# Kernel optimization log

Measured on AMD Instinct MI355X. Metric: run time of the kernel, lower is better.

Reference implementation:

```python
import jax, jax.numpy as jnp
import numpy as np

D = 256; NH = 8; NL = 4; NP = 4; NLAYERS = 6; DFF = 1024; DH = D // NH
B = 2
SHAPES = [(128, 128), (64, 64), (32, 32), (16, 16)]
S_TOTAL = sum(h * w for h, w in SHAPES)  # 21760


def setup_inputs() -> dict:
    key = jax.random.key(0)
    ks = iter(jax.random.split(key, 64))
    inp = {}
    for l, (h, w) in enumerate(SHAPES):
        inp[f"src{l}"] = jax.random.normal(next(ks), (B, D, h, w), jnp.float32)
        inp[f"pos{l}"] = jax.random.normal(next(ks), (B, D, h, w), jnp.float32)
    def p(shape):
        return jax.random.normal(next(ks), shape, jnp.float32) * 0.02
    inp["level_embed"] = p((NL, D))
    inp["Woff"] = p((NLAYERS, D, NH * NL * NP * 2)); inp["boff"] = p((NLAYERS, NH * NL * NP * 2))
    inp["Wattn"] = p((NLAYERS, D, NH * NL * NP)); inp["battn"] = p((NLAYERS, NH * NL * NP))
    inp["Wval"] = p((NLAYERS, D, D)); inp["bval"] = p((NLAYERS, D))
    inp["Wout"] = p((NLAYERS, D, D)); inp["bout"] = p((NLAYERS, D))
    inp["ln1_s"] = jnp.ones((NLAYERS, D)); inp["ln1_b"] = jnp.zeros((NLAYERS, D))
    inp["W1"] = p((NLAYERS, D, DFF)); inp["b1"] = p((NLAYERS, DFF))
    inp["W2"] = p((NLAYERS, DFF, D)); inp["b2"] = p((NLAYERS, D))
    inp["ln2_s"] = jnp.ones((NLAYERS, D)); inp["ln2_b"] = jnp.zeros((NLAYERS, D))
    return inp


def _layer_norm(x, s, b, eps=1e-5):
    m = jnp.mean(x, -1, keepdims=True)
    v = jnp.mean((x - m) ** 2, -1, keepdims=True)
    return (x - m) * jax.lax.rsqrt(v + eps) * s + b


def _ref_points(batch):
    # masks are all-False -> valid_ratios == 1, so reference points are just
    # normalized pixel centers, identical across the level axis.
    refs = []
    for h, w in SHAPES:
        yy, xx = jnp.meshgrid((jnp.arange(h) + 0.5) / h, (jnp.arange(w) + 0.5) / w, indexing="ij")
        refs.append(jnp.stack([xx.ravel(), yy.ravel()], -1))
    ref = jnp.concatenate(refs, 0)  # [S, 2] (x, y)
    return jnp.broadcast_to(ref[None, :, None, :], (batch, S_TOTAL, NL, 2))


def _ms_deform_attn(query, ref, src, Woff, boff, Wattn, battn, Wval, bval, Wout, bout):
    Bq, S, _ = query.shape
    value = (src @ Wval + bval).reshape(Bq, S, NH, DH)
    off = (query @ Woff + boff).reshape(Bq, S, NH, NL, NP, 2)
    aw = jax.nn.softmax((query @ Wattn + battn).reshape(Bq, S, NH, NL * NP), -1)
    aw = aw.reshape(Bq, S, NH, NL, NP)
    norm = jnp.array([[w, h] for h, w in SHAPES], dtype=query.dtype)  # [NL,2] = (W,H)
    loc = ref[:, :, None, :, None, :] + off / norm[None, None, None, :, None, :]  # [B,S,NH,NL,NP,2]
    out = jnp.zeros((Bq, NH, S, DH), query.dtype)
    start = 0
    for l, (h, w) in enumerate(SHAPES):
        v = value[:, start:start + h * w].transpose(0, 2, 1, 3)  # [B,NH,h*w,DH]
        start += h * w
        # grid_sample align_corners=False convention
        x = loc[:, :, :, l, :, 0] * w - 0.5  # [B,S,NH,NP]
        y = loc[:, :, :, l, :, 1] * h - 0.5
        x0 = jnp.floor(x); y0 = jnp.floor(y)
        lx = x - x0; ly = y - y0
        x0i = x0.astype(jnp.int32); y0i = y0.astype(jnp.int32)
        def tr(a):  # [B,S,NH,NP] -> [B,NH,S*NP,1]
            return a.transpose(0, 2, 1, 3).reshape(Bq, NH, S * NP, 1)
        def gather(xi, yi):
            ok = (xi >= 0) & (xi < w) & (yi >= 0) & (yi < h)
            idx = jnp.clip(yi, 0, h - 1) * w + jnp.clip(xi, 0, w - 1)
            idx = idx.transpose(0, 2, 1, 3).reshape(Bq, NH, S * NP)
            g = jnp.take_along_axis(v, idx[..., None], axis=2)  # [B,NH,S*NP,DH]
            return g * tr(ok).astype(v.dtype)  # zero padding outside
        samp = (tr((1 - lx) * (1 - ly)) * gather(x0i, y0i)
                + tr(lx * (1 - ly)) * gather(x0i + 1, y0i)
                + tr((1 - lx) * ly) * gather(x0i, y0i + 1)
                + tr(lx * ly) * gather(x0i + 1, y0i + 1))
        samp = (samp * tr(aw[:, :, :, l])).reshape(Bq, NH, S, NP, DH).sum(3)
        out = out + samp
    out = out.transpose(0, 2, 1, 3).reshape(Bq, S, D)
    return out @ Wout + bout


def _forward(srcs, poss, level_embed, Woff, boff, Wattn, battn, Wval, bval, Wout, bout,
             ln1_s, ln1_b, W1, b1, W2, b2, ln2_s, ln2_b):
    bsz = srcs[0].shape[0]
    src_flat = jnp.concatenate([s.reshape(bsz, D, -1).transpose(0, 2, 1) for s in srcs], 1)
    pos_flat = jnp.concatenate(
        [p.reshape(bsz, D, -1).transpose(0, 2, 1) + level_embed[l] for l, p in enumerate(poss)], 1)
    ref = _ref_points(bsz)
    out = src_flat
    for i in range(NLAYERS):
        q = out + pos_flat
        attn = _ms_deform_attn(q, ref, out, Woff[i], boff[i], Wattn[i], battn[i],
                               Wval[i], bval[i], Wout[i], bout[i])
        out = _layer_norm(out + attn, ln1_s[i], ln1_b[i])
        ff = jax.nn.relu(out @ W1[i] + b1[i]) @ W2[i] + b2[i]
        out = _layer_norm(out + ff, ln2_s[i], ln2_b[i])
    return out  # memory: [B, S_TOTAL, D]


def reference(src0, src1, src2, src3, pos0, pos1, pos2, pos3, level_embed,
              Woff, boff, Wattn, battn, Wval, bval, Wout, bout,
              ln1_s, ln1_b, W1, b1, W2, b2, ln2_s, ln2_b):
    return _forward([src0, src1, src2, src3], [pos0, pos1, pos2, pos3], level_embed,
                    Woff, boff, Wattn, battn, Wval, bval, Wout, bout,
                    ln1_s, ln1_b, W1, b1, W2, b2, ln2_s, ln2_b)
```

## Files before the change

### kernel.cpp

```cpp
#include <hip/hip_runtime.h>
#include <math.h>

#define DMODEL 256
#define NHEADS 8
#define NLAY 6
#define DFF 1024
#define DHEAD 32
#define NB 2
#define STOT 21760
#define MTOT (NB * STOT)

typedef unsigned short u16;
typedef __attribute__((ext_vector_type(8))) short short8;
typedef __attribute__((ext_vector_type(4))) float floatx4;
typedef __attribute__((ext_vector_type(2))) float float2v;

__device__ __forceinline__ float bf2f(u16 h) {
    unsigned int u = ((unsigned int)h) << 16;
    return __uint_as_float(u);
}
__device__ __forceinline__ u16 f2bf(float f) {
    unsigned int u = __float_as_uint(f);
    u = u + 0x7fffu + ((u >> 16) & 1u);
    return (u16)(u >> 16);
}

__device__ __forceinline__ void pkfma(float2v& acc, float2v a, float2v b) {
    asm("v_pk_fma_f32 %0, %1, %2, %0" : "+v"(acc) : "v"(a), "v"(b));
}
__device__ __forceinline__ float2v unpk(unsigned int u) {
    float2v r;
    r.x = __uint_as_float(u << 16);
    r.y = __uint_as_float(u & 0xffff0000u);
    return r;
}

__device__ __forceinline__ void gload16(const u16* g, u16* l) {
    __builtin_amdgcn_global_load_lds(
        (const __attribute__((address_space(1))) unsigned int*)(g),
        (__attribute__((address_space(3))) unsigned int*)(l),
        16, 0, 0);
}

__global__ __launch_bounds__(256)
void biascat_kernel(const float* __restrict__ boff, const float* __restrict__ battn,
                    float* __restrict__ bias384)
{
    const int t = blockIdx.x * 256 + threadIdx.x;
    if (t >= NLAY * 384) return;
    const int i = t / 384, c = t - i * 384;
    bias384[t] = (c < 256) ? boff[i * 256 + c] : battn[i * 128 + (c - 256)];
}

__global__ __launch_bounds__(256)
void wtrans_kernel(const float* __restrict__ W, u16* __restrict__ Wt,
                   const int K, const int N, const long wstride, const long ostride)
{
    __shared__ float ts[32][33];
    W  += blockIdx.z * wstride;
    Wt += blockIdx.z * ostride;
    const int n0 = blockIdx.x * 32;
    const int k0 = blockIdx.y * 32;
    const int t = threadIdx.x;
    const int nl = t & 31, kl = t >> 5;
#pragma unroll
    for (int p = 0; p < 4; ++p) {
        const int k = kl + p * 8;
        ts[k][nl] = W[(long)(k0 + k) * N + n0 + nl];
    }
    __syncthreads();
    const int c = t & 31, r0 = t >> 5;
#pragma unroll
    for (int p = 0; p < 4; ++p) {
        const int r = r0 + p * 8;
        Wt[(long)(n0 + r) * K + k0 + c] = f2bf(ts[c][r]);
    }
}

__global__ __launch_bounds__(256)
void flatten_kernel(const float* __restrict__ src, const float* __restrict__ pos,
                    const float* __restrict__ le_row,
                    float* __restrict__ out, u16* __restrict__ outb,
                    u16* __restrict__ posb, u16* __restrict__ qb,
                    int HW, int start)
{
    __shared__ float ts[32][33];
    __shared__ float tp[32][33];
    const int b   = blockIdx.z;
    const int d0  = blockIdx.y * 32;
    const int hw0 = blockIdx.x * 32;
    const int t   = threadIdx.x;
    const int hwl = t & 31;
    const int dl  = t >> 5;
#pragma unroll
    for (int p = 0; p < 4; ++p) {
        const int dd = dl + p * 8;
        const int d  = d0 + dd;
        const long idx = ((long)(b * DMODEL + d)) * HW + hw0 + hwl;
        ts[dd][hwl] = src[idx];
        tp[dd][hwl] = pos[idx] + le_row[d];
    }
    __syncthreads();
    const int dl2  = t & 31;
    const int hwl2 = t >> 5;
#pragma unroll
    for (int p = 0; p < 4; ++p) {
        const int hh  = hwl2 + p * 8;
        const int tok = start + hw0 + hh;
        const long o  = ((long)(b * STOT + tok)) * DMODEL + d0 + dl2;
        const float v = ts[dl2][hh];
        const float pp = tp[dl2][hh];
        out[o]  = v;
        outb[o] = f2bf(v);
        posb[o] = f2bf(pp);
        qb[o]   = f2bf(v + pp);
    }
}

__global__ __launch_bounds__(256)
void mfma_gemm(const u16* __restrict__ A, const u16* __restrict__ Bt,
               const int ldb, const float* __restrict__ bias,
               u16* __restrict__ Cb, const int ldc, u16* __restrict__ Cb2,
               const int K, const int relu)
{
    __shared__ u16 As[2][128 * 32];
    __shared__ u16 Bs[2][128 * 32];
    const int tid  = threadIdx.x;
    const int wv   = tid >> 6;
    const int lane = tid & 63;
    const int m0 = blockIdx.y * 128;
    const int n0 = blockIdx.x * 128;
    const int wm = (wv & 1) * 64;
    const int wn = (wv >> 1) * 64;
    const int q   = lane >> 4;
    const int c16 = lane & 15;

    const int lrow = lane >> 2;
    const int lcol = (lane & 3) * 8;

    const u16* ag[2];
    const u16* bg[2];
#pragma unroll
    for (int it = 0; it < 2; ++it) {
        const int chunk = it * 4 + wv;
        const int row = chunk * 16 + lrow;
        ag[it] = A  + (long)(m0 + row) * K   + lcol;
        bg[it] = Bt + (long)(n0 + row) * ldb + lcol;
    }

#define STAGE(buf, kk)                                          \
    {                                                           \
        _Pragma("unroll")                                       \
        for (int it = 0; it < 2; ++it) {                        \
            const int chunk = it * 4 + wv;                      \
            gload16(ag[it] + (kk), &As[buf][chunk * 512]);      \
            gload16(bg[it] + (kk), &Bs[buf][chunk * 512]);      \
        }                                                       \
    }

    floatx4 acc[4][4];
#pragma unroll
    for (int i = 0; i < 4; ++i)
#pragma unroll
        for (int j = 0; j < 4; ++j)
            acc[i][j] = (floatx4){0.f, 0.f, 0.f, 0.f};

    STAGE(0, 0);
    __syncthreads();

    int cur = 0;
    for (int k0 = 0; k0 < K; k0 += 32) {
        const int nxt = k0 + 32;
        if (nxt < K) {
            if (cur) { STAGE(0, nxt); } else { STAGE(1, nxt); }
        }

        const u16* Ab = &As[cur][0];
        const u16* Bb = &Bs[cur][0];
        short8 af[4], bf[4];
#pragma unroll
        for (int i = 0; i < 4; ++i) {
            af[i] = *(const short8*)&Ab[(wm + i * 16 + c16) * 32 + q * 8];
            bf[i] = *(const short8*)&Bb[(wn + i * 16 + c16) * 32 + q * 8];
        }
#pragma unroll
        for (int i = 0; i < 4; ++i)
#pragma unroll
            for (int j = 0; j < 4; ++j)
                acc[i][j] = __builtin_amdgcn_mfma_f32_16x16x32_bf16(
                    af[i], bf[j], acc[i][j], 0, 0, 0);
        __syncthreads();
        cur ^= 1;
    }
#undef STAGE

    u16* cb  = Cb;
    int ldcb = ldc, csub = 0;
    if (Cb2 && n0 >= 256) { cb = Cb2; ldcb = 128; csub = 256; }

#pragma unroll
    for (int i = 0; i < 4; ++i) {
#pragma unroll
        for (int j = 0; j < 4; ++j) {
            const int col = n0 + wn + j * 16 + c16;
            const float bv = bias ? bias[col] : 0.f;
#pragma unroll
            for (int r = 0; r < 4; ++r) {
                const int row = m0 + wm + i * 16 + q * 4 + r;
                float v = acc[i][j][r] + bv;
                if (relu) v = fmaxf(v, 0.f);
                cb[(long)row * ldcb + col - csub] = f2bf(v);
            }
        }
    }
}

__device__ __forceinline__ void point_corners(
    float refx, float refy, unsigned int o2, float aP,
    int k, unsigned int base, float* w, unsigned int* o)
{
    const int lw = 128 >> k;
    const float flw = (float)lw;
    const float x = refx * flw - 0.5f + bf2f((u16)(o2 & 0xffffu));
    const float y = refy * flw - 0.5f + bf2f((u16)(o2 >> 16));
    const float x0f = floorf(x), y0f = floorf(y);
    const float lx = x - x0f, ly = y - y0f;
    const int x0 = (int)x0f, y0 = (int)y0f;
    const float wx0 = ((unsigned int)x0 < (unsigned int)lw) ? (1.f - lx) : 0.f;
    const float wx1 = ((unsigned int)(x0 + 1) < (unsigned int)lw) ? lx : 0.f;
    const float wy0 = ((unsigned int)y0 < (unsigned int)lw) ? (aP * (1.f - ly)) : 0.f;
    const float wy1 = ((unsigned int)(y0 + 1) < (unsigned int)lw) ? (aP * ly) : 0.f;
    const unsigned int xc0 = (unsigned int)(x0 & (lw - 1)) << 9;
    const unsigned int xc1 = (unsigned int)((x0 + 1) & (lw - 1)) << 9;
    const unsigned int r0 = (unsigned int)(y0 & (lw - 1)) << (16 - k);
    const unsigned int r1 = (unsigned int)((y0 + 1) & (lw - 1)) << (16 - k);
    w[0] = wy0 * wx0; o[0] = base + r0 + xc0;
    w[1] = wy0 * wx1; o[1] = base + r0 + xc1;
    w[2] = wy1 * wx0; o[2] = base + r1 + xc0;
    w[3] = wy1 * wx1; o[3] = base + r1 + xc1;
}

__global__ __launch_bounds__(256, 4)
void sample_kernel(const u16* __restrict__ value, const u16* __restrict__ offb,
                   const u16* __restrict__ logit, u16* __restrict__ sb)
{
    __shared__ unsigned int pwtab[4 * 8 * 132];

    const int t  = threadIdx.x;
    const int wv = t >> 6;
    const int l  = t & 63;
    const int h  = l >> 3;
    const int u  = l & 7;
    const int blk = blockIdx.x * 4 + wv;
    const int b = blk / STOT;
    const int s = blk - b * STOT;

    float refx, refy;
    if (s < 16384) {
        const int yy = s >> 7, xx = s & 127;
        refx = (xx + 0.5f) * (1.f / 128.f); refy = (yy + 0.5f) * (1.f / 128.f);
    } else if (s < 20480) {
        const int sl = s - 16384; const int yy = sl >> 6, xx = sl & 63;
        refx = (xx + 0.5f) * (1.f / 64.f);  refy = (yy + 0.5f) * (1.f / 64.f);
    } else if (s < 21504) {
        const int sl = s - 20480; const int yy = sl >> 5, xx = sl & 31;
        refx = (xx + 0.5f) * (1.f / 32.f);  refy = (yy + 0.5f) * (1.f / 32.f);
    } else {
        const int sl = s - 21504; const int yy = sl >> 4, xx = sl & 15;
        refx = (xx + 0.5f) * (1.f / 16.f);  refy = (yy + 0.5f) * (1.f / 16.f);
    }

    const unsigned int* offp = (const unsigned int*)(offb + (long)blk * 256 + h * 32);
    const unsigned int o2_0 = offp[u];
    const unsigned int o2_1 = offp[u + 8];
    const u16* lp = logit + (long)blk * 128 + h * 16;
    const float l0 = bf2f(lp[u]);
    const float l1 = bf2f(lp[u + 8]);

    float m = fmaxf(l0, l1);
    m = fmaxf(m, __shfl_xor(m, 1));
    m = fmaxf(m, __shfl_xor(m, 2));
    m = fmaxf(m, __shfl_xor(m, 4));
    const float e0 = __expf(l0 - m);
    const float e1 = __expf(l1 - m);
    float se = e0 + e1;
    se += __shfl_xor(se, 1);
    se += __shfl_xor(se, 2);
    se += __shfl_xor(se, 4);
    const float inv = 1.f / se;
    const float aP0 = e0 * inv;
    const float aP1 = e1 * inv;

    const int k0 = u >> 2;
    const unsigned int LS0 = k0 ? 16384u : 0u;
    const unsigned int LS1 = k0 ? 21504u : 20480u;
    const unsigned int tb = (unsigned int)(b * STOT);
    const unsigned int hb64 = (unsigned int)(h * 64);
    const unsigned int base0 = (tb + LS0) * 512u + hb64;
    const unsigned int base1 = (tb + LS1) * 512u + hb64;

    float ww[8];
    unsigned int oo[8];
    point_corners(refx, refy, o2_0, aP0, k0,     base0, ww,     oo);
    point_corners(refx, refy, o2_1, aP1, k0 + 2, base1, ww + 4, oo + 4);

    unsigned int* wbase = pwtab + (wv * 8 + h) * 132;
    {
        uint4 p0, p1, p2, p3;
        p0.x = __float_as_uint(ww[0]); p0.y = oo[0];
        p0.z = __float_as_uint(ww[1]); p0.w = oo[1];
        p1.x = __float_as_uint(ww[2]); p1.y = oo[2];
        p1.z = __float_as_uint(ww[3]); p1.w = oo[3];
        p2.x = __float_as_uint(ww[4]); p2.y = oo[4];
        p2.z = __float_as_uint(ww[5]); p2.w = oo[5];
        p3.x = __float_as_uint(ww[6]); p3.y = oo[6];
        p3.z = __float_as_uint(ww[7]); p3.w = oo[7];
        *(uint4*)(wbase + u * 8)           = p0;
        *(uint4*)(wbase + u * 8 + 4)       = p1;
        *(uint4*)(wbase + (u + 8) * 8)     = p2;
        *(uint4*)(wbase + (u + 8) * 8 + 4) = p3;
    }
    __builtin_amdgcn_wave_barrier();

    const unsigned int chb = (unsigned int)(u * 8);
    const char* vp = (const char*)value;
    float2v acc0; acc0.x = 0.f; acc0.y = 0.f;
    float2v acc1; acc1.x = 0.f; acc1.y = 0.f;

#pragma unroll
    for (int g = 0; g < 4; ++g) {
        const uint4* gp = (const uint4*)(wbase + g * 32);
        uint4 qq[8];
#pragma unroll
        for (int i = 0; i < 8; ++i) qq[i] = gp[i];
        uint2 dB[16];
#pragma unroll
        for (int i = 0; i < 8; ++i) {
            dB[2 * i]     = *(const uint2*)(vp + (qq[i].y + chb));
            dB[2 * i + 1] = *(const uint2*)(vp + (qq[i].w + chb));
        }
#pragma unroll
        for (int i = 0; i < 8; ++i) {
            float2v wa; wa.x = __uint_as_float(qq[i].x); wa.y = wa.x;
            pkfma(acc0, wa, unpk(dB[2 * i].x));
            pkfma(acc1, wa, unpk(dB[2 * i].y));
            float2v wb; wb.x = __uint_as_float(qq[i].z); wb.y = wb.x;
            pkfma(acc0, wb, unpk(dB[2 * i + 1].x));
            pkfma(acc1, wb, unpk(dB[2 * i + 1].y));
        }
    }

    ushort4 r;
    r.x = f2bf(acc0.x); r.y = f2bf(acc0.y);
    r.z = f2bf(acc1.x); r.w = f2bf(acc1.y);
    *(ushort4*)(sb + (long)blk * DMODEL + h * 32 + u * 4) = r;
}

__global__ __launch_bounds__(256)
void ln_kernel(float* __restrict__ out, u16* __restrict__ outb,
               u16* __restrict__ qb, const u16* __restrict__ posb,
               const u16* __restrict__ db,
               const float* __restrict__ gamma, const float* __restrict__ beta)
{
    const int wave = threadIdx.x >> 6;
    const int lane = threadIdx.x & 63;
    const long tok = (long)blockIdx.x * 4 + wave;
    float* op = out + tok * DMODEL + lane * 4;
    const float4 xo = *(const float4*)op;
    const ushort4 d4 = *(const ushort4*)(db + tok * DMODEL + lane * 4);
    float x[4] = {xo.x + bf2f(d4.x), xo.y + bf2f(d4.y),
                  xo.z + bf2f(d4.z), xo.w + bf2f(d4.w)};

    float sum = x[0] + x[1] + x[2] + x[3];
#pragma unroll
    for (int o = 32; o >= 1; o >>= 1) sum += __shfl_xor(sum, o);
    const float mean = sum * (1.f / 256.f);

    float vs = 0.f;
#pragma unroll
    for (int i = 0; i < 4; ++i) { const float d2 = x[i] - mean; vs += d2 * d2; }
#pragma unroll
    for (int o = 32; o >= 1; o >>= 1) vs += __shfl_xor(vs, o);
    const float rstd = rsqrtf(vs * (1.f / 256.f) + 1e-5f);

    const float4 g  = *(const float4*)(gamma + lane * 4);
    const float4 be = *(const float4*)(beta + lane * 4);
    float r[4];
    r[0] = (x[0] - mean) * rstd * g.x + be.x;
    r[1] = (x[1] - mean) * rstd * g.y + be.y;
    r[2] = (x[2] - mean) * rstd * g.z + be.z;
    r[3] = (x[3] - mean) * rstd * g.w + be.w;
    float4 rf; rf.x = r[0]; rf.y = r[1]; rf.z = r[2]; rf.w = r[3];
    *(float4*)op = rf;
    ushort4 rb;
    rb.x = f2bf(r[0]); rb.y = f2bf(r[1]); rb.z = f2bf(r[2]); rb.w = f2bf(r[3]);
    *(ushort4*)(outb + tok * DMODEL + lane * 4) = rb;
    if (qb) {
        const ushort4 p4 = *(const ushort4*)(posb + tok * DMODEL + lane * 4);
        ushort4 qv;
        qv.x = f2bf(r[0] + bf2f(p4.x));
        qv.y = f2bf(r[1] + bf2f(p4.y));
        qv.z = f2bf(r[2] + bf2f(p4.z));
        qv.w = f2bf(r[3] + bf2f(p4.w));
        *(ushort4*)(qb + tok * DMODEL + lane * 4) = qv;
    }
}

extern "C" void kernel_launch(void* const* d_in, const int* in_sizes, int n_in,
                              void* d_out, int out_size, void* d_ws, size_t ws_size,
                              hipStream_t stream)
{
    const float* src[4] = {(const float*)d_in[0], (const float*)d_in[2],
                           (const float*)d_in[4], (const float*)d_in[6]};
    const float* pos[4] = {(const float*)d_in[1], (const float*)d_in[3],
                           (const float*)d_in[5], (const float*)d_in[7]};
    const float* level_embed = (const float*)d_in[8];
    const float* Woff  = (const float*)d_in[9];
    const float* boff  = (const float*)d_in[10];
    const float* Wattn = (const float*)d_in[11];
    const float* battn = (const float*)d_in[12];
    const float* Wval  = (const float*)d_in[13];
    const float* bval  = (const float*)d_in[14];
    const float* Wout  = (const float*)d_in[15];
    const float* bout  = (const float*)d_in[16];
    const float* ln1s  = (const float*)d_in[17];
    const float* ln1b  = (const float*)d_in[18];
    const float* W1    = (const float*)d_in[19];
    const float* b1    = (const float*)d_in[20];
    const float* W2    = (const float*)d_in[21];
    const float* b2    = (const float*)d_in[22];
    const float* ln2s  = (const float*)d_in[23];
    const float* ln2b  = (const float*)d_in[24];

    float* out = (float*)d_out;
    const long MD = (long)MTOT * DMODEL;

    u16* outb = (u16*)d_ws;
    u16* posb = outb + MD;
    u16* qb   = posb + MD;
    u16* db   = qb + MD;
    u16* vb   = db + MD;
    u16* offb = vb + MD;
    u16* awb  = offb + MD;
    u16* sb   = awb + MD / 2;
    u16* hb   = vb;
    u16* wts  = vb + 4 * MD;
    u16* Wvalt = wts;
    u16* Wofat = Wvalt + 6L * 256 * 256;
    u16* Woutt = Wofat + 6L * 384 * 256;
    u16* W1t   = Woutt + 6L * 256 * 256;
    u16* W2t   = W1t   + 6L * 1024 * 256;
    float* bias384 = (float*)(W2t + 6L * 1024 * 256);

    biascat_kernel<<<9, 256, 0, stream>>>(boff, battn, bias384);
    wtrans_kernel<<<dim3(8, 8, 6),  256, 0, stream>>>(Wval,  Wvalt, 256, 256,
                                                      65536, 65536);
    wtrans_kernel<<<dim3(8, 8, 6),  256, 0, stream>>>(Woff,  Wofat, 256, 256,
                                                      65536, 98304);
    wtrans_kernel<<<dim3(4, 8, 6),  256, 0, stream>>>(Wattn, Wofat + 256 * 256,
                                                      256, 128, 32768, 98304);
    wtrans_kernel<<<dim3(8, 8, 6),  256, 0, stream>>>(Wout,  Woutt, 256, 256,
                                                      65536, 65536);
    wtrans_kernel<<<dim3(32, 8, 6), 256, 0, stream>>>(W1,    W1t, 256, 1024,
                                                      262144, 262144);
    wtrans_kernel<<<dim3(8, 32, 6), 256, 0, stream>>>(W2,    W2t, 1024, 256,
                                                      262144, 262144);

    {
        const int HW[4] = {16384, 4096, 1024, 256};
        const int ST[4] = {0, 16384, 20480, 21504};
        for (int l = 0; l < 4; ++l) {
            dim3 g(HW[l] / 32, DMODEL / 32, NB);
            flatten_kernel<<<g, 256, 0, stream>>>(src[l], pos[l],
                                                  level_embed + l * DMODEL,
                                                  out, outb, posb, qb, HW[l], ST[l]);
        }
    }

    const dim3 g2(2, MTOT / 128);
    const dim3 g3(3, MTOT / 128);
    const dim3 g8(8, MTOT / 128);

    for (int i = 0; i < NLAY; ++i) {
        const u16* Wv  = Wvalt + (long)i * 256 * 256;
        const u16* Wqa = Wofat + (long)i * 384 * 256;
        const u16* Wou = Woutt + (long)i * 256 * 256;
        const u16* W1i = W1t   + (long)i * 1024 * 256;
        const u16* W2i = W2t   + (long)i * 256 * 1024;
        const float* bv  = bval + (long)i * 256;
        const float* bqa = bias384 + (long)i * 384;
        const float* bou = bout + (long)i * 256;
        const float* b1i = b1   + (long)i * DFF;
        const float* b2i = b2   + (long)i * 256;

        mfma_gemm<<<g2, 256, 0, stream>>>(outb, Wv, 256, bv,
                                          vb, 256, nullptr, 256, 0);
        mfma_gemm<<<g3, 256, 0, stream>>>(qb, Wqa, 256, bqa,
                                          offb, 256, awb, 256, 0);
        sample_kernel<<<MTOT / 4, 256, 0, stream>>>(vb, offb, awb, sb);
        mfma_gemm<<<g2, 256, 0, stream>>>(sb, Wou, 256, bou,
                                          db, 256, nullptr, 256, 0);
        ln_kernel<<<MTOT / 4, 256, 0, stream>>>(out, outb, nullptr, nullptr, db,
                                                ln1s + (long)i * 256,
                                                ln1b + (long)i * 256);
        mfma_gemm<<<g8, 256, 0, stream>>>(outb, W1i, 256, b1i,
                                          hb, 1024, nullptr, 256, 1);
        mfma_gemm<<<g2, 256, 0, stream>>>(hb, W2i, 1024, b2i,
                                          db, 256, nullptr, 1024, 0);
        ln_kernel<<<MTOT / 4, 256, 0, stream>>>(out, outb, qb, posb, db,
                                                ln2s + (long)i * 256,
                                                ln2b + (long)i * 256);
    }
}
```

Measured before the change: 1.900 ms.

## Merge value and offset GEMMs into one launch; software-pipeline sampling gathers

The value projection and the offset/attention-logit projection now run as a single grouped GEMM launch: blocks with column index past a split point switch to the second operand set. This removes one launch per layer and fills the GPU better with 5 column tiles instead of 2 and 3. The sampling kernel double-buffers its gather loads so the next group's value loads are in flight while the current group is accumulated, with sched_barriers enforcing the order. This raises register use, so occupancy is lowered from 4 to 3 blocks per CU.

```diff
diff --git a/kernel.cpp b/kernel.cpp
--- a/kernel.cpp
+++ b/kernel.cpp
@@ -121,15 +121,22 @@
 void mfma_gemm(const u16* __restrict__ A, const u16* __restrict__ Bt,
                const int ldb, const float* __restrict__ bias,
                u16* __restrict__ Cb, const int ldc, u16* __restrict__ Cb2,
-               const int K, const int relu)
+               const int K, const int relu,
+               const u16* __restrict__ A1, const u16* __restrict__ Bt1,
+               const float* __restrict__ bias1, u16* __restrict__ Cb1,
+               u16* __restrict__ Cb21, const int nsplit)
 {
     __shared__ u16 As[2][128 * 32];
     __shared__ u16 Bs[2][128 * 32];
+    int bx = blockIdx.x;
+    if (A1 && bx >= nsplit) {
+        A = A1; Bt = Bt1; bias = bias1; Cb = Cb1; Cb2 = Cb21; bx -= nsplit;
+    }
     const int tid  = threadIdx.x;
     const int wv   = tid >> 6;
     const int lane = tid & 63;
     const int m0 = blockIdx.y * 128;
-    const int n0 = blockIdx.x * 128;
+    const int n0 = bx * 128;
     const int wm = (wv & 1) * 64;
     const int wn = (wv >> 1) * 64;
     const int q   = lane >> 4;
@@ -240,7 +247,34 @@
     w[3] = wy1 * wx1; o[3] = base + r1 + xc1;
 }
 
-__global__ __launch_bounds__(256, 4)
+#define LDQ(Q, g)                                                   \
+    {                                                               \
+        const uint4* gp_ = (const uint4*)(wbase + (g) * 32);        \
+        _Pragma("unroll")                                           \
+        for (int i = 0; i < 8; ++i) Q[i] = gp_[i];                  \
+    }
+#define GATH(D, Q)                                                  \
+    {                                                               \
+        _Pragma("unroll")                                           \
+        for (int i = 0; i < 8; ++i) {                               \
+            D[2 * i]     = *(const uint2*)(vp + (Q[i].y + chb));    \
+            D[2 * i + 1] = *(const uint2*)(vp + (Q[i].w + chb));    \
+        }                                                           \
+    }
+#define FMAG(D, Q)                                                  \
+    {                                                               \
+        _Pragma("unroll")                                           \
+        for (int i = 0; i < 8; ++i) {                               \
+            float2v wa; wa.x = __uint_as_float(Q[i].x); wa.y = wa.x;\
+            pkfma(acc0, wa, unpk(D[2 * i].x));                      \
+            pkfma(acc1, wa, unpk(D[2 * i].y));                      \
+            float2v wb; wb.x = __uint_as_float(Q[i].z); wb.y = wb.x;\
+            pkfma(acc0, wb, unpk(D[2 * i + 1].x));                  \
+            pkfma(acc1, wb, unpk(D[2 * i + 1].y));                  \
+        }                                                           \
+    }
+
+__global__ __launch_bounds__(256, 3)
 void sample_kernel(const u16* __restrict__ value, const u16* __restrict__ offb,
                    const u16* __restrict__ logit, u16* __restrict__ sb)
 {
@@ -327,28 +361,23 @@
     float2v acc0; acc0.x = 0.f; acc0.y = 0.f;
     float2v acc1; acc1.x = 0.f; acc1.y = 0.f;
 
-#pragma unroll
-    for (int g = 0; g < 4; ++g) {
-        const uint4* gp = (const uint4*)(wbase + g * 32);
-        uint4 qq[8];
-#pragma unroll
-        for (int i = 0; i < 8; ++i) qq[i] = gp[i];
-        uint2 dB[16];
-#pragma unroll
-        for (int i = 0; i < 8; ++i) {
-            dB[2 * i]     = *(const uint2*)(vp + (qq[i].y + chb));
-            dB[2 * i + 1] = *(const uint2*)(vp + (qq[i].w + chb));
-        }
-#pragma unroll
-        for (int i = 0; i < 8; ++i) {
-            float2v wa; wa.x = __uint_as_float(qq[i].x); wa.y = wa.x;
-            pkfma(acc0, wa, unpk(dB[2 * i].x));
-            pkfma(acc1, wa, unpk(dB[2 * i].y));
-            float2v wb; wb.x = __uint_as_float(qq[i].z); wb.y = wb.x;
-            pkfma(acc0, wb, unpk(dB[2 * i + 1].x));
-            pkfma(acc1, wb, unpk(dB[2 * i + 1].y));
-        }
-    }
+    uint4 qA[8], qB[8];
+    uint2 dA[16], dB[16];
+
+    LDQ(qA, 0); GATH(dA, qA);
+    LDQ(qB, 1); GATH(dB, qB);
+    __builtin_amdgcn_sched_barrier(0);
+    FMAG(dA, qA);
+    __builtin_amdgcn_sched_barrier(0);
+    LDQ(qA, 2); GATH(dA, qA);
+    __builtin_amdgcn_sched_barrier(0);
+    FMAG(dB, qB);
+    __builtin_amdgcn_sched_barrier(0);
+    LDQ(qB, 3); GATH(dB, qB);
+    __builtin_amdgcn_sched_barrier(0);
+    FMAG(dA, qA);
+    __builtin_amdgcn_sched_barrier(0);
+    FMAG(dB, qB);
 
     ushort4 r;
     r.x = f2bf(acc0.x); r.y = f2bf(acc0.y);
@@ -478,7 +507,7 @@
     }
 
     const dim3 g2(2, MTOT / 128);
-    const dim3 g3(3, MTOT / 128);
+    const dim3 g5(5, MTOT / 128);
     const dim3 g8(8, MTOT / 128);
 
     for (int i = 0; i < NLAY; ++i) {
@@ -493,20 +522,25 @@
         const float* b1i = b1   + (long)i * DFF;
         const float* b2i = b2   + (long)i * 256;
 
-        mfma_gemm<<<g2, 256, 0, stream>>>(outb, Wv, 256, bv,
-                                          vb, 256, nullptr, 256, 0);
-        mfma_gemm<<<g3, 256, 0, stream>>>(qb, Wqa, 256, bqa,
-                                          offb, 256, awb, 256, 0);
+        mfma_gemm<<<g5, 256, 0, stream>>>(outb, Wv, 256, bv,
+                                          vb, 256, nullptr, 256, 0,
+                                          qb, Wqa, bqa, offb, awb, 2);
         sample_kernel<<<MTOT / 4, 256, 0, stream>>>(vb, offb, awb, sb);
         mfma_gemm<<<g2, 256, 0, stream>>>(sb, Wou, 256, bou,
-                                          db, 256, nullptr, 256, 0);
+                                          db, 256, nullptr, 256, 0,
+                                          nullptr, nullptr, nullptr, nullptr,
+                                          nullptr, 0);
         ln_kernel<<<MTOT / 4, 256, 0, stream>>>(out, outb, nullptr, nullptr, db,
                                                 ln1s + (long)i * 256,
                                                 ln1b + (long)i * 256);
         mfma_gemm<<<g8, 256, 0, stream>>>(outb, W1i, 256, b1i,
-                                          hb, 1024, nullptr, 256, 1);
+                                          hb, 1024, nullptr, 256, 1,
+                                          nullptr, nullptr, nullptr, nullptr,
+                                          nullptr, 0);
         mfma_gemm<<<g2, 256, 0, stream>>>(hb, W2i, 1024, b2i,
-                                          db, 256, nullptr, 1024, 0);
+                                          db, 256, nullptr, 1024, 0,
+                                          nullptr, nullptr, nullptr, nullptr,
+                                          nullptr, 0);
         ln_kernel<<<MTOT / 4, 256, 0, stream>>>(out, outb, qb, posb, db,
                                                 ln2s + (long)i * 256,
                                                 ln2b + (long)i * 256);
```

Result: faster. 1.861 ms (-2.1%).

## Triple-buffer GEMM k-loop with single barrier and merge value/offset GEMM launches

Applied to the files above, without the earlier changes.

The GEMM main loop moves from double to triple buffering. It keeps two stages of async global-to-LDS loads in flight, uses explicit vmcnt waits, and needs only one barrier per k-step. The kernel also gains a second operand set selected by block x index, so the value projection and the offset/attention projection run in one launch. This raises LDS use per block, which may lower occupancy, and adds hand-written waitcnt assembly that depends on the load count per stage.

```diff
diff --git a/kernel.cpp b/kernel.cpp
--- a/kernel.cpp
+++ b/kernel.cpp
@@ -121,15 +121,22 @@
 void mfma_gemm(const u16* __restrict__ A, const u16* __restrict__ Bt,
                const int ldb, const float* __restrict__ bias,
                u16* __restrict__ Cb, const int ldc, u16* __restrict__ Cb2,
-               const int K, const int relu)
-{
-    __shared__ u16 As[2][128 * 32];
-    __shared__ u16 Bs[2][128 * 32];
+               const int K, const int relu,
+               const u16* __restrict__ A1, const u16* __restrict__ Bt1,
+               const float* __restrict__ bias1, u16* __restrict__ Cb1,
+               u16* __restrict__ Cb21, const int nsplit)
+{
+    __shared__ u16 As[3][128 * 32];
+    __shared__ u16 Bs[3][128 * 32];
+    int bx = blockIdx.x;
+    if (A1 && bx >= nsplit) {
+        A = A1; Bt = Bt1; bias = bias1; Cb = Cb1; Cb2 = Cb21; bx -= nsplit;
+    }
     const int tid  = threadIdx.x;
     const int wv   = tid >> 6;
     const int lane = tid & 63;
     const int m0 = blockIdx.y * 128;
-    const int n0 = blockIdx.x * 128;
+    const int n0 = bx * 128;
     const int wm = (wv & 1) * 64;
     const int wn = (wv >> 1) * 64;
     const int q   = lane >> 4;
@@ -165,14 +172,24 @@
         for (int j = 0; j < 4; ++j)
             acc[i][j] = (floatx4){0.f, 0.f, 0.f, 0.f};
 
+    const int nk = K >> 5;
     STAGE(0, 0);
-    __syncthreads();
+    STAGE(1, 32);
 
     int cur = 0;
-    for (int k0 = 0; k0 < K; k0 += 32) {
-        const int nxt = k0 + 32;
-        if (nxt < K) {
-            if (cur) { STAGE(0, nxt); } else { STAGE(1, nxt); }
+    for (int k = 0; k < nk; ++k) {
+        __builtin_amdgcn_sched_barrier(0);
+        if (k < nk - 1) {
+            asm volatile("s_waitcnt vmcnt(4) lgkmcnt(0)" ::: "memory");
+        } else {
+            asm volatile("s_waitcnt vmcnt(0) lgkmcnt(0)" ::: "memory");
+        }
+        __builtin_amdgcn_s_barrier();
+        __builtin_amdgcn_sched_barrier(0);
+
+        if (k + 2 < nk) {
+            const int nb = (cur + 2 >= 3) ? (cur - 1) : (cur + 2);
+            STAGE(nb, (k + 2) * 32);
         }
 
         const u16* Ab = &As[cur][0];
@@ -189,8 +206,8 @@
             for (int j = 0; j < 4; ++j)
                 acc[i][j] = __builtin_amdgcn_mfma_f32_16x16x32_bf16(
                     af[i], bf[j], acc[i][j], 0, 0, 0);
-        __syncthreads();
-        cur ^= 1;
+
+        cur = (cur == 2) ? 0 : (cur + 1);
     }
 #undef STAGE
 
@@ -478,7 +495,7 @@
     }
 
     const dim3 g2(2, MTOT / 128);
-    const dim3 g3(3, MTOT / 128);
+    const dim3 g5(5, MTOT / 128);
     const dim3 g8(8, MTOT / 128);
 
     for (int i = 0; i < NLAY; ++i) {
@@ -493,20 +510,25 @@
         const float* b1i = b1   + (long)i * DFF;
         const float* b2i = b2   + (long)i * 256;
 
-        mfma_gemm<<<g2, 256, 0, stream>>>(outb, Wv, 256, bv,
-                                          vb, 256, nullptr, 256, 0);
-        mfma_gemm<<<g3, 256, 0, stream>>>(qb, Wqa, 256, bqa,
-                                          offb, 256, awb, 256, 0);
+        mfma_gemm<<<g5, 256, 0, stream>>>(outb, Wv, 256, bv,
+                                          vb, 256, nullptr, 256, 0,
+                                          qb, Wqa, bqa, offb, awb, 2);
         sample_kernel<<<MTOT / 4, 256, 0, stream>>>(vb, offb, awb, sb);
         mfma_gemm<<<g2, 256, 0, stream>>>(sb, Wou, 256, bou,
-                                          db, 256, nullptr, 256, 0);
+                                          db, 256, nullptr, 256, 0,
+                                          nullptr, nullptr, nullptr, nullptr,
+                                          nullptr, 0);
         ln_kernel<<<MTOT / 4, 256, 0, stream>>>(out, outb, nullptr, nullptr, db,
                                                 ln1s + (long)i * 256,
                                                 ln1b + (long)i * 256);
         mfma_gemm<<<g8, 256, 0, stream>>>(outb, W1i, 256, b1i,
-                                          hb, 1024, nullptr, 256, 1);
+                                          hb, 1024, nullptr, 256, 1,
+                                          nullptr, nullptr, nullptr, nullptr,
+                                          nullptr, 0);
         mfma_gemm<<<g2, 256, 0, stream>>>(hb, W2i, 1024, b2i,
-                                          db, 256, nullptr, 1024, 0);
+                                          db, 256, nullptr, 1024, 0,
+                                          nullptr, nullptr, nullptr, nullptr,
+                                          nullptr, 0);
         ln_kernel<<<MTOT / 4, 256, 0, stream>>>(out, outb, qb, posb, db,
                                                 ln2s + (long)i * 256,
                                                 ln2b + (long)i * 256);
```

New measurement: 1.922 ms. Within noise of the previous version (+1.2%).

## Fuse residual LayerNorm into output GEMMs and merge value/offset GEMM launches

Applied to the files above, without the earlier changes.

Adds a GEMM kernel with 64-row by 256-column tiles. Each block covers a full model row, so the bias, residual add and LayerNorm (with an optional pos-add query output) run in the epilogue. This removes the separate ln_kernel launches and the round trip of the intermediate bf16 delta buffer. The value and offset/attention projections are also merged into one launch by splitting blockIdx.x between two operand sets. The cost is fewer, larger GEMM tiles with more registers per thread, a variance taken as E[x^2]-mean^2, and scalar rather than vectorized epilogue stores.

```diff
diff --git a/kernel.cpp b/kernel.cpp
--- a/kernel.cpp
+++ b/kernel.cpp
@@ -121,15 +121,22 @@
 void mfma_gemm(const u16* __restrict__ A, const u16* __restrict__ Bt,
                const int ldb, const float* __restrict__ bias,
                u16* __restrict__ Cb, const int ldc, u16* __restrict__ Cb2,
-               const int K, const int relu)
+               const int K, const int relu,
+               const u16* __restrict__ A1, const u16* __restrict__ Bt1,
+               const float* __restrict__ bias1, u16* __restrict__ Cb1,
+               u16* __restrict__ Cb21, const int nsplit)
 {
     __shared__ u16 As[2][128 * 32];
     __shared__ u16 Bs[2][128 * 32];
+    int bx = blockIdx.x;
+    if (A1 && bx >= nsplit) {
+        A = A1; Bt = Bt1; bias = bias1; Cb = Cb1; Cb2 = Cb21; bx -= nsplit;
+    }
     const int tid  = threadIdx.x;
     const int wv   = tid >> 6;
     const int lane = tid & 63;
     const int m0 = blockIdx.y * 128;
-    const int n0 = blockIdx.x * 128;
+    const int n0 = bx * 128;
     const int wm = (wv & 1) * 64;
     const int wn = (wv >> 1) * 64;
     const int q   = lane >> 4;
@@ -210,6 +217,164 @@
                 float v = acc[i][j][r] + bv;
                 if (relu) v = fmaxf(v, 0.f);
                 cb[(long)row * ldcb + col - csub] = f2bf(v);
+            }
+        }
+    }
+}
+
+__global__ __launch_bounds__(256, 3)
+void gemmln_kernel(const u16* __restrict__ A, const u16* __restrict__ Bt,
+                   const float* __restrict__ bias,
+                   float* __restrict__ out, u16* __restrict__ outb,
+                   u16* __restrict__ qb, const u16* __restrict__ posb,
+                   const float* __restrict__ gamma, const float* __restrict__ beta,
+                   const int K)
+{
+    __shared__ u16 As[2][64 * 32];
+    __shared__ u16 Bs[2][256 * 32];
+    const int tid  = threadIdx.x;
+    const int wv   = tid >> 6;
+    const int lane = tid & 63;
+    const int m0 = blockIdx.x * 64;
+    const int wm  = (wv & 1) * 32;
+    const int wn  = (wv >> 1) * 128;
+    const int q   = lane >> 4;
+    const int c16 = lane & 15;
+
+    const int lrow = lane >> 2;
+    const int lcol = (lane & 3) * 8;
+
+    const u16* ag = A + (long)(m0 + wv * 16 + lrow) * K + lcol;
+    const u16* bg[4];
+#pragma unroll
+    for (int p = 0; p < 4; ++p)
+        bg[p] = Bt + (long)(p * 64 + wv * 16 + lrow) * K + lcol;
+
+#define STAGE(buf, kk)                                              \
+    {                                                               \
+        gload16(ag + (kk), &As[buf][(wv * 16) * 32]);               \
+        _Pragma("unroll")                                           \
+        for (int p = 0; p < 4; ++p)                                 \
+            gload16(bg[p] + (kk), &Bs[buf][(p * 64 + wv * 16) * 32]); \
+    }
+
+    floatx4 acc[2][8];
+#pragma unroll
+    for (int i = 0; i < 2; ++i)
+#pragma unroll
+        for (int j = 0; j < 8; ++j)
+            acc[i][j] = (floatx4){0.f, 0.f, 0.f, 0.f};
+
+    STAGE(0, 0);
+    __syncthreads();
+
+    int cur = 0;
+    for (int k0 = 0; k0 < K; k0 += 32) {
+        const int nxt = k0 + 32;
+        if (nxt < K) {
+            if (cur) { STAGE(0, nxt); } else { STAGE(1, nxt); }
+        }
+
+        const u16* Ab = &As[cur][0];
+        const u16* Bb = &Bs[cur][0];
+        short8 af[2], bf[8];
+#pragma unroll
+        for (int i = 0; i < 2; ++i)
+            af[i] = *(const short8*)&Ab[(wm + i * 16 + c16) * 32 + q * 8];
+#pragma unroll
+        for (int j = 0; j < 8; ++j)
+            bf[j] = *(const short8*)&Bb[(wn + j * 16 + c16) * 32 + q * 8];
+#pragma unroll
+        for (int i = 0; i < 2; ++i)
+#pragma unroll
+            for (int j = 0; j < 8; ++j)
+                acc[i][j] = __builtin_amdgcn_mfma_f32_16x16x32_bf16(
+                    af[i], bf[j], acc[i][j], 0, 0, 0);
+        __syncthreads();
+        cur ^= 1;
+    }
+#undef STAGE
+
+    float bc[8], gc[8], ec[8];
+#pragma unroll
+    for (int j = 0; j < 8; ++j) {
+        const int c = wn + j * 16 + c16;
+        bc[j] = bias[c];
+        gc[j] = gamma[c];
+        ec[j] = beta[c];
+    }
+
+    float s1[2][4], s2[2][4];
+#pragma unroll
+    for (int i = 0; i < 2; ++i) {
+#pragma unroll
+        for (int r = 0; r < 4; ++r) {
+            const long token = (long)m0 + wm + i * 16 + q * 4 + r;
+            const float* op = out + token * DMODEL;
+            float a = 0.f, b2 = 0.f;
+#pragma unroll
+            for (int j = 0; j < 8; ++j) {
+                float v = acc[i][j][r] + bc[j] + op[wn + j * 16 + c16];
+                acc[i][j][r] = v;
+                a += v;
+                b2 = fmaf(v, v, b2);
+            }
+#pragma unroll
+            for (int o = 1; o <= 8; o <<= 1) {
+                a  += __shfl_xor(a, o);
+                b2 += __shfl_xor(b2, o);
+            }
+            s1[i][r] = a;
+            s2[i][r] = b2;
+        }
+    }
+
+    float* red = (float*)&As[0][0];
+    if (c16 == 0) {
+        const int half = wn >> 7;
+#pragma unroll
+        for (int i = 0; i < 2; ++i)
+#pragma unroll
+            for (int r = 0; r < 4; ++r) {
+                const int rl = wm + i * 16 + q * 4 + r;
+                float2v v; v.x = s1[i][r]; v.y = s2[i][r];
+                *(float2v*)&red[rl * 4 + half * 2] = v;
+            }
+    }
+    __syncthreads();
+
+    float mean[2][4], rstd[2][4];
+#pragma unroll
+    for (int i = 0; i < 2; ++i)
+#pragma unroll
+        for (int r = 0; r < 4; ++r) {
+            const int rl = wm + i * 16 + q * 4 + r;
+            const float4 v = *(const float4*)&red[rl * 4];
+            const float m_  = (v.x + v.z) * (1.f / 256.f);
+            const float e2  = (v.y + v.w) * (1.f / 256.f);
+            const float var = fmaxf(e2 - m_ * m_, 0.f);
+            mean[i][r] = m_;
+            rstd[i][r] = rsqrtf(var + 1e-5f);
+        }
+
+#pragma unroll
+    for (int i = 0; i < 2; ++i) {
+#pragma unroll
+        for (int r = 0; r < 4; ++r) {
+            const long token = (long)m0 + wm + i * 16 + q * 4 + r;
+            const float m_ = mean[i][r];
+            const float rs = rstd[i][r];
+            float* op  = out  + token * DMODEL;
+            u16*   ob  = outb + token * DMODEL;
+            u16*   qp  = qb   ? qb   + token * DMODEL : nullptr;
+            const u16* pp = posb ? posb + token * DMODEL : nullptr;
+#pragma unroll
+            for (int j = 0; j < 8; ++j) {
+                const int c = wn + j * 16 + c16;
+                const float y = (acc[i][j][r] - m_) * rs * gc[j] + ec[j];
+                op[c] = y;
+                ob[c] = f2bf(y);
+                if (qp) qp[c] = f2bf(y + bf2f(pp[c]));
             }
         }
     }
@@ -354,56 +519,6 @@
     r.x = f2bf(acc0.x); r.y = f2bf(acc0.y);
     r.z = f2bf(acc1.x); r.w = f2bf(acc1.y);
     *(ushort4*)(sb + (long)blk * DMODEL + h * 32 + u * 4) = r;
-}
-
-__global__ __launch_bounds__(256)
-void ln_kernel(float* __restrict__ out, u16* __restrict__ outb,
-               u16* __restrict__ qb, const u16* __restrict__ posb,
-               const u16* __restrict__ db,
-               const float* __restrict__ gamma, const float* __restrict__ beta)
-{
-    const int wave = threadIdx.x >> 6;
-    const int lane = threadIdx.x & 63;
-    const long tok = (long)blockIdx.x * 4 + wave;
-    float* op = out + tok * DMODEL + lane * 4;
-    const float4 xo = *(const float4*)op;
-    const ushort4 d4 = *(const ushort4*)(db + tok * DMODEL + lane * 4);
-    float x[4] = {xo.x + bf2f(d4.x), xo.y + bf2f(d4.y),
-                  xo.z + bf2f(d4.z), xo.w + bf2f(d4.w)};
-
-    float sum = x[0] + x[1] + x[2] + x[3];
-#pragma unroll
-    for (int o = 32; o >= 1; o >>= 1) sum += __shfl_xor(sum, o);
-    const float mean = sum * (1.f / 256.f);
-
-    float vs = 0.f;
-#pragma unroll
-    for (int i = 0; i < 4; ++i) { const float d2 = x[i] - mean; vs += d2 * d2; }
-#pragma unroll
-    for (int o = 32; o >= 1; o >>= 1) vs += __shfl_xor(vs, o);
-    const float rstd = rsqrtf(vs * (1.f / 256.f) + 1e-5f);
-
-    const float4 g  = *(const float4*)(gamma + lane * 4);
-    const float4 be = *(const float4*)(beta + lane * 4);
-    float r[4];
-    r[0] = (x[0] - mean) * rstd * g.x + be.x;
-    r[1] = (x[1] - mean) * rstd * g.y + be.y;
-    r[2] = (x[2] - mean) * rstd * g.z + be.z;
-    r[3] = (x[3] - mean) * rstd * g.w + be.w;
-    float4 rf; rf.x = r[0]; rf.y = r[1]; rf.z = r[2]; rf.w = r[3];
-    *(float4*)op = rf;
-    ushort4 rb;
-    rb.x = f2bf(r[0]); rb.y = f2bf(r[1]); rb.z = f2bf(r[2]); rb.w = f2bf(r[3]);
-    *(ushort4*)(outb + tok * DMODEL + lane * 4) = rb;
-    if (qb) {
-        const ushort4 p4 = *(const ushort4*)(posb + tok * DMODEL + lane * 4);
-        ushort4 qv;
-        qv.x = f2bf(r[0] + bf2f(p4.x));
-        qv.y = f2bf(r[1] + bf2f(p4.y));
-        qv.z = f2bf(r[2] + bf2f(p4.z));
-        qv.w = f2bf(r[3] + bf2f(p4.w));
-        *(ushort4*)(qb + tok * DMODEL + lane * 4) = qv;
-    }
 }
 
 extern "C" void kernel_launch(void* const* d_in, const int* in_sizes, int n_in,
@@ -477,8 +592,7 @@
         }
     }
 
-    const dim3 g2(2, MTOT / 128);
-    const dim3 g3(3, MTOT / 128);
+    const dim3 g5(5, MTOT / 128);
     const dim3 g8(8, MTOT / 128);
 
     for (int i = 0; i < NLAY; ++i) {
@@ -493,22 +607,21 @@
         const float* b1i = b1   + (long)i * DFF;
         const float* b2i = b2   + (long)i * 256;
 
-        mfma_gemm<<<g2, 256, 0, stream>>>(outb, Wv, 256, bv,
-                                          vb, 256, nullptr, 256, 0);
-        mfma_gemm<<<g3, 256, 0, stream>>>(qb, Wqa, 256, bqa,
-                                          offb, 256, awb, 256, 0);
+        mfma_gemm<<<g5, 256, 0, stream>>>(outb, Wv, 256, bv,
+                                          vb, 256, nullptr, 256, 0,
+                                          qb, Wqa, bqa, offb, awb, 2);
         sample_kernel<<<MTOT / 4, 256, 0, stream>>>(vb, offb, awb, sb);
-        mfma_gemm<<<g2, 256, 0, stream>>>(sb, Wou, 256, bou,
-                                          db, 256, nullptr, 256, 0);
-        ln_kernel<<<MTOT / 4, 256, 0, stream>>>(out, outb, nullptr, nullptr, db,
-                                                ln1s + (long)i * 256,
-                                                ln1b + (long)i * 256);
+        gemmln_kernel<<<MTOT / 64, 256, 0, stream>>>(sb, Wou, bou,
+                                                     out, outb, nullptr, nullptr,
+                                                     ln1s + (long)i * 256,
+                                                     ln1b + (long)i * 256, 256);
         mfma_gemm<<<g8, 256, 0, stream>>>(outb, W1i, 256, b1i,
-                                          hb, 1024, nullptr, 256, 1);
-        mfma_gemm<<<g2, 256, 0, stream>>>(hb, W2i, 1024, b2i,
-                                          db, 256, nullptr, 1024, 0);
-        ln_kernel<<<MTOT / 4, 256, 0, stream>>>(out, outb, qb, posb, db,
-                                                ln2s + (long)i * 256,
-                                                ln2b + (long)i * 256);
-    }
-}
+                                          hb, 1024, nullptr, 256, 1,
+                                          nullptr, nullptr, nullptr, nullptr,
+                                          nullptr, 0);
+        gemmln_kernel<<<MTOT / 64, 256, 0, stream>>>(hb, W2i, b2i,
+                                                     out, outb, qb, posb,
+                                                     ln2s + (long)i * 256,
+                                                     ln2b + (long)i * 256, 1024);
+    }
+}
```

New measurement: 1.833 ms. 1.04x faster.
